# Optimization experiments

Measured on AMD Instinct MI355X. Metric: run time of the kernel, lower is better.

The kernel has to match this reference:

```python
import jax, jax.numpy as jnp
import numpy as np

MARGIN = 0.3


def setup_inputs() -> dict:
    key = jax.random.key(0)
    k1, k2 = jax.random.split(key)
    embeddings = jax.random.normal(k1, (4096, 128), dtype=jnp.float32)
    labels = jax.random.randint(k2, (4096,), 0, 256, dtype=jnp.int64)
    return {"embeddings": embeddings, "labels": labels}


def reference(embeddings, labels):
    # L2-normalize rows (same as F.normalize(p=2, dim=1), eps=1e-12)
    norm = jnp.maximum(jnp.linalg.norm(embeddings, axis=1, keepdims=True), 1e-12)
    e = embeddings / norm
    # cosine distance matrix [N, N]
    dist = 1.0 - e @ e.T

    same = labels[None, :] == labels[:, None]          # [N, N]
    n = labels.shape[0]
    eye = jnp.eye(n, dtype=bool)
    pos_mask = same & ~eye                             # positives excl. self
    neg_mask = ~same

    # dist in [0, 2]; finite sentinels keep max/min well-defined per row
    hardest_pos = jnp.max(jnp.where(pos_mask, dist, -1.0), axis=1)
    hardest_neg = jnp.min(jnp.where(neg_mask, dist, 3.0), axis=1)

    valid = jnp.any(pos_mask, axis=1) & jnp.any(neg_mask, axis=1)
    per_row = jax.nn.relu(hardest_pos - hardest_neg + MARGIN)
    loss_sum = jnp.sum(jnp.where(valid, per_row, 0.0))
    count = jnp.sum(valid)
    return loss_sum / jnp.maximum(count, 1).astype(loss_sum.dtype)
```

## Files before the change

### kernel.cpp

```cpp
#include <hip/hip_runtime.h>
#include <stdint.h>

typedef __bf16 bf16x8 __attribute__((ext_vector_type(8)));
typedef float f32x4 __attribute__((ext_vector_type(4)));

#define N_ROWS 4096
#define KD 128
#define BM 64
#define NCHUNK 16
#define CHUNK 256
#define NBLOCKS (64 * NCHUNK)

__device__ __forceinline__ unsigned short f32_to_bf16_rne(float f) {
    union { float f; uint32_t u; } v; v.f = f;
    uint32_t u = v.u;
    return (unsigned short)((u + 0x7FFFu + ((u >> 16) & 1u)) >> 16);
}

__device__ __forceinline__ int swz(int row, int c) { return row * 16 + (c ^ (row & 15)); }
__device__ __forceinline__ int swzL(int L) { return (L & ~15) | ((L & 15) ^ ((L >> 4) & 15)); }

__global__ __launch_bounds__(256) void normalize_kernel(const float* __restrict__ E,
                                                        unsigned short* __restrict__ out) {
    const int wave = threadIdx.x >> 6;
    const int lane = threadIdx.x & 63;
    const int row = blockIdx.x * 4 + wave;
    const float2 v = *(const float2*)&E[row * KD + lane * 2];
    float s = v.x * v.x + v.y * v.y;
#pragma unroll
    for (int m = 1; m < 64; m <<= 1) s += __shfl_xor(s, m, 64);
    float inv = 0.0f;
    if (s > 0.0f) {
        inv = rsqrtf(s);
        inv = inv * (1.5f - 0.5f * s * inv * inv);
    }
    const unsigned short a = f32_to_bf16_rne(v.x * inv);
    const unsigned short b = f32_to_bf16_rne(v.y * inv);
    ((uint32_t*)out)[row * (KD / 2) + lane] = ((uint32_t)b << 16) | a;
}

__global__ __launch_bounds__(256, 2) void gram_kernel(const unsigned short* __restrict__ Ebits,
                                                      const int* __restrict__ labels,
                                                      float2* __restrict__ partials) {
    __shared__ uint4 Bs4[CHUNK * (KD / 8)];
    __shared__ int ljs[CHUNK];

    const int tid = threadIdx.x;
    const int itile = blockIdx.x & 63;
    const int chunk = blockIdx.x >> 6;
    const int ibase = itile * BM;
    const int cbase = chunk * CHUNK;

    const int wave = tid >> 6, lane = tid & 63;
    const int quad = lane >> 4, l15 = lane & 15;
    const int igb = ibase + wave * 16 + quad * 4;

    uint4 breg[16];
    {
        const uint4* bsrc = (const uint4*)(Ebits + (size_t)cbase * KD);
#pragma unroll
        for (int it = 0; it < 16; ++it) breg[it] = bsrc[it * 256 + tid];
    }
    ljs[tid] = labels[cbase + tid];

    bf16x8 afrag[4];
    {
        const uint4* asrc = (const uint4*)Ebits;
        const int arow = ibase + wave * 16 + l15;
#pragma unroll
        for (int s = 0; s < 4; ++s) afrag[s] = *(const bf16x8*)&asrc[arow * 16 + s * 4 + quad];
    }
    int li_lab[4];
#pragma unroll
    for (int r = 0; r < 4; ++r) li_lab[r] = labels[igb + r];

#pragma unroll
    for (int it = 0; it < 16; ++it) Bs4[swzL(it * 256 + tid)] = breg[it];
    __syncthreads();

    float minpos[4] = {2.0f, 2.0f, 2.0f, 2.0f};
    float maxneg[4] = {-2.0f, -2.0f, -2.0f, -2.0f};

#pragma unroll 4
    for (int t = 0; t < 16; ++t) {
        f32x4 acc = {0.f, 0.f, 0.f, 0.f};
#pragma unroll
        for (int s = 0; s < 4; ++s) {
            const bf16x8 bfrag = *(const bf16x8*)&Bs4[swz(t * 16 + l15, s * 4 + quad)];
            acc = __builtin_amdgcn_mfma_f32_16x16x32_bf16(afrag[s], bfrag, acc, 0, 0, 0);
        }
        const int jg = cbase + t * 16 + l15;
        const int lj = ljs[t * 16 + l15];
#pragma unroll
        for (int r = 0; r < 4; ++r) {
            const float d = acc[r];
            const bool same = (lj == li_lab[r]);
            const float dp = (same && (igb + r != jg)) ? d : 2.0f;
            const float dn = same ? -2.0f : d;
            minpos[r] = fminf(minpos[r], dp);
            maxneg[r] = fmaxf(maxneg[r], dn);
        }
    }

#pragma unroll
    for (int m = 1; m < 16; m <<= 1) {
#pragma unroll
        for (int r = 0; r < 4; ++r) {
            minpos[r] = fminf(minpos[r], __shfl_xor(minpos[r], m, 64));
            maxneg[r] = fmaxf(maxneg[r], __shfl_xor(maxneg[r], m, 64));
        }
    }
    if (l15 == 0) {
#pragma unroll
        for (int r = 0; r < 4; ++r)
            partials[(igb + r) * NCHUNK + chunk] = make_float2(minpos[r], maxneg[r]);
    }
}

__global__ __launch_bounds__(256) void finalize_kernel(const float2* __restrict__ partials,
                                                       float* __restrict__ out) {
    __shared__ float ssum[4];
    __shared__ int scnt[4];
    float sum = 0.f;
    int cnt = 0;
    for (int row = threadIdx.x; row < N_ROWS; row += 256) {
        float mp = 2.f, mn = -2.f;
        const float4* p4 = (const float4*)&partials[row * NCHUNK];
#pragma unroll
        for (int c = 0; c < NCHUNK / 2; ++c) {
            const float4 v = p4[c];
            mp = fminf(mp, fminf(v.x, v.z));
            mn = fmaxf(mn, fmaxf(v.y, v.w));
        }
        if (mp < 1.5f && mn > -1.5f) {
            sum += fmaxf(0.f, mn - mp + 0.3f);
            cnt += 1;
        }
    }
#pragma unroll
    for (int m = 1; m < 64; m <<= 1) {
        sum += __shfl_xor(sum, m, 64);
        cnt += __shfl_xor(cnt, m, 64);
    }
    const int wave = threadIdx.x >> 6, lane = threadIdx.x & 63;
    if (lane == 0) { ssum[wave] = sum; scnt[wave] = cnt; }
    __syncthreads();
    if (threadIdx.x == 0) {
        const float S = ssum[0] + ssum[1] + ssum[2] + ssum[3];
        const int C = scnt[0] + scnt[1] + scnt[2] + scnt[3];
        out[0] = S / (float)(C > 0 ? C : 1);
    }
}

extern "C" void kernel_launch(void* const* d_in, const int* in_sizes, int n_in,
                              void* d_out, int out_size, void* d_ws, size_t ws_size,
                              hipStream_t stream) {
    const float* E = (const float*)d_in[0];
    const int* labels = (const int*)d_in[1];

    unsigned short* ebits = (unsigned short*)d_ws;
    float2* partials = (float2*)((char*)d_ws + (size_t)N_ROWS * KD * 2);
    float* out = (float*)d_out;

    normalize_kernel<<<N_ROWS / 4, 256, 0, stream>>>(E, ebits);
    gram_kernel<<<NBLOCKS, 256, 0, stream>>>(ebits, labels, partials);
    finalize_kernel<<<1, 256, 0, stream>>>(partials, out);
}
```

Baseline: 83.51 us.

## Tile gram B-chunk through small LDS buffer and parallelize finalize across blocks

The gram kernel now stages the A tile in LDS and streams the 256-row B chunk in four 64-row sub-tiles through a smaller shared buffer, replacing the 64KB register-staged chunk. This cuts LDS use per block and register pressure, so more blocks can be resident, at the cost of extra barriers and no overlap between loads and MFMAs. The finalize step moves from a single block to 64 blocks. Each block reduces its rows and combines results through global atomics, and a ticket counter lets the last block write the mean. The atomic counters are reset in the normalize kernel.

```diff
diff --git a/kernel.cpp b/kernel.cpp
--- a/kernel.cpp
+++ b/kernel.cpp
@@ -7,9 +7,12 @@
 #define N_ROWS 4096
 #define KD 128
 #define BM 64
+#define BN 64
 #define NCHUNK 16
 #define CHUNK 256
+#define JT (CHUNK / BN)
 #define NBLOCKS (64 * NCHUNK)
+#define FIN_BLOCKS 64
 
 __device__ __forceinline__ unsigned short f32_to_bf16_rne(float f) {
     union { float f; uint32_t u; } v; v.f = f;
@@ -21,7 +24,13 @@
 __device__ __forceinline__ int swzL(int L) { return (L & ~15) | ((L & 15) ^ ((L >> 4) & 15)); }
 
 __global__ __launch_bounds__(256) void normalize_kernel(const float* __restrict__ E,
-                                                        unsigned short* __restrict__ out) {
+                                                        unsigned short* __restrict__ out,
+                                                        float* __restrict__ gsum,
+                                                        unsigned* __restrict__ gcnt,
+                                                        unsigned* __restrict__ ticket) {
+    if (blockIdx.x == 0 && threadIdx.x == 0) {
+        *gsum = 0.0f; *gcnt = 0u; *ticket = 0u;
+    }
     const int wave = threadIdx.x >> 6;
     const int lane = threadIdx.x & 63;
     const int row = blockIdx.x * 4 + wave;
@@ -39,10 +48,11 @@
     ((uint32_t*)out)[row * (KD / 2) + lane] = ((uint32_t)b << 16) | a;
 }
 
-__global__ __launch_bounds__(256, 2) void gram_kernel(const unsigned short* __restrict__ Ebits,
-                                                      const int* __restrict__ labels,
-                                                      float2* __restrict__ partials) {
-    __shared__ uint4 Bs4[CHUNK * (KD / 8)];
+__global__ __launch_bounds__(256) void gram_kernel(const unsigned short* __restrict__ Ebits,
+                                                   const int* __restrict__ labels,
+                                                   float2* __restrict__ partials) {
+    __shared__ uint4 As4[BM * KD / 8];
+    __shared__ uint4 Bs4[BN * KD / 8];
     __shared__ int ljs[CHUNK];
 
     const int tid = threadIdx.x;
@@ -51,54 +61,65 @@
     const int ibase = itile * BM;
     const int cbase = chunk * CHUNK;
 
+    {
+        const uint4* src = (const uint4*)(Ebits + (size_t)ibase * KD);
+#pragma unroll
+        for (int it = 0; it < 4; ++it) {
+            const int L = it * 256 + tid;
+            As4[swzL(L)] = src[L];
+        }
+        ljs[tid] = labels[cbase + tid];
+    }
+    __syncthreads();
+
     const int wave = tid >> 6, lane = tid & 63;
     const int quad = lane >> 4, l15 = lane & 15;
     const int igb = ibase + wave * 16 + quad * 4;
 
-    uint4 breg[16];
-    {
-        const uint4* bsrc = (const uint4*)(Ebits + (size_t)cbase * KD);
-#pragma unroll
-        for (int it = 0; it < 16; ++it) breg[it] = bsrc[it * 256 + tid];
-    }
-    ljs[tid] = labels[cbase + tid];
-
     bf16x8 afrag[4];
-    {
-        const uint4* asrc = (const uint4*)Ebits;
-        const int arow = ibase + wave * 16 + l15;
-#pragma unroll
-        for (int s = 0; s < 4; ++s) afrag[s] = *(const bf16x8*)&asrc[arow * 16 + s * 4 + quad];
-    }
+#pragma unroll
+    for (int s = 0; s < 4; ++s)
+        afrag[s] = *(const bf16x8*)&As4[swz(wave * 16 + l15, s * 4 + quad)];
+
     int li_lab[4];
 #pragma unroll
     for (int r = 0; r < 4; ++r) li_lab[r] = labels[igb + r];
-
-#pragma unroll
-    for (int it = 0; it < 16; ++it) Bs4[swzL(it * 256 + tid)] = breg[it];
-    __syncthreads();
 
     float minpos[4] = {2.0f, 2.0f, 2.0f, 2.0f};
     float maxneg[4] = {-2.0f, -2.0f, -2.0f, -2.0f};
 
-#pragma unroll 4
-    for (int t = 0; t < 16; ++t) {
-        f32x4 acc = {0.f, 0.f, 0.f, 0.f};
-#pragma unroll
-        for (int s = 0; s < 4; ++s) {
-            const bf16x8 bfrag = *(const bf16x8*)&Bs4[swz(t * 16 + l15, s * 4 + quad)];
-            acc = __builtin_amdgcn_mfma_f32_16x16x32_bf16(afrag[s], bfrag, acc, 0, 0, 0);
-        }
-        const int jg = cbase + t * 16 + l15;
-        const int lj = ljs[t * 16 + l15];
-#pragma unroll
-        for (int r = 0; r < 4; ++r) {
-            const float d = acc[r];
-            const bool same = (lj == li_lab[r]);
-            const float dp = (same && (igb + r != jg)) ? d : 2.0f;
-            const float dn = same ? -2.0f : d;
-            minpos[r] = fminf(minpos[r], dp);
-            maxneg[r] = fmaxf(maxneg[r], dn);
+    for (int jt = 0; jt < JT; ++jt) {
+        const int jbase = cbase + jt * BN;
+        __syncthreads();
+        {
+            const uint4* src = (const uint4*)(Ebits + (size_t)jbase * KD);
+#pragma unroll
+            for (int it = 0; it < 4; ++it) {
+                const int L = it * 256 + tid;
+                Bs4[swzL(L)] = src[L];
+            }
+        }
+        __syncthreads();
+
+#pragma unroll
+        for (int t = 0; t < 4; ++t) {
+            f32x4 acc = {0.f, 0.f, 0.f, 0.f};
+#pragma unroll
+            for (int s = 0; s < 4; ++s) {
+                const bf16x8 bfrag = *(const bf16x8*)&Bs4[swz(t * 16 + l15, s * 4 + quad)];
+                acc = __builtin_amdgcn_mfma_f32_16x16x32_bf16(afrag[s], bfrag, acc, 0, 0, 0);
+            }
+            const int jg = jbase + t * 16 + l15;
+            const int lj = ljs[jt * BN + t * 16 + l15];
+#pragma unroll
+            for (int r = 0; r < 4; ++r) {
+                const float d = acc[r];
+                const bool same = (lj == li_lab[r]);
+                const float dp = (same && (igb + r != jg)) ? d : 2.0f;
+                const float dn = same ? -2.0f : d;
+                minpos[r] = fminf(minpos[r], dp);
+                maxneg[r] = fmaxf(maxneg[r], dn);
+            }
         }
     }
 
@@ -118,37 +139,50 @@
 }
 
 __global__ __launch_bounds__(256) void finalize_kernel(const float2* __restrict__ partials,
+                                                       float* __restrict__ gsum,
+                                                       unsigned* __restrict__ gcnt,
+                                                       unsigned* __restrict__ ticket,
                                                        float* __restrict__ out) {
     __shared__ float ssum[4];
     __shared__ int scnt[4];
-    float sum = 0.f;
-    int cnt = 0;
-    for (int row = threadIdx.x; row < N_ROWS; row += 256) {
-        float mp = 2.f, mn = -2.f;
-        const float4* p4 = (const float4*)&partials[row * NCHUNK];
-#pragma unroll
-        for (int c = 0; c < NCHUNK / 2; ++c) {
-            const float4 v = p4[c];
-            mp = fminf(mp, fminf(v.x, v.z));
-            mn = fmaxf(mn, fmaxf(v.y, v.w));
-        }
-        if (mp < 1.5f && mn > -1.5f) {
-            sum += fmaxf(0.f, mn - mp + 0.3f);
-            cnt += 1;
-        }
+    __shared__ unsigned s_old;
+
+    const int tid = threadIdx.x;
+    const int sub = tid & 3;
+    const int row = blockIdx.x * 64 + (tid >> 2);
+
+    const float4* p4 = (const float4*)&partials[row * NCHUNK];
+    const float4 a = p4[sub * 2];
+    const float4 b = p4[sub * 2 + 1];
+    float mp = fminf(fminf(a.x, a.z), fminf(b.x, b.z));
+    float mn = fmaxf(fmaxf(a.y, a.w), fmaxf(b.y, b.w));
+    mp = fminf(mp, __shfl_xor(mp, 1, 64)); mp = fminf(mp, __shfl_xor(mp, 2, 64));
+    mn = fmaxf(mn, __shfl_xor(mn, 1, 64)); mn = fmaxf(mn, __shfl_xor(mn, 2, 64));
+
+    float sum = 0.f; int cnt = 0;
+    if (sub == 0 && mp < 1.5f && mn > -1.5f) {
+        sum = fmaxf(0.f, mn - mp + 0.3f);
+        cnt = 1;
     }
 #pragma unroll
     for (int m = 1; m < 64; m <<= 1) {
         sum += __shfl_xor(sum, m, 64);
         cnt += __shfl_xor(cnt, m, 64);
     }
-    const int wave = threadIdx.x >> 6, lane = threadIdx.x & 63;
+    const int wave = tid >> 6, lane = tid & 63;
     if (lane == 0) { ssum[wave] = sum; scnt[wave] = cnt; }
     __syncthreads();
-    if (threadIdx.x == 0) {
-        const float S = ssum[0] + ssum[1] + ssum[2] + ssum[3];
-        const int C = scnt[0] + scnt[1] + scnt[2] + scnt[3];
-        out[0] = S / (float)(C > 0 ? C : 1);
+    if (tid == 0) {
+        atomicAdd(gsum, ssum[0] + ssum[1] + ssum[2] + ssum[3]);
+        atomicAdd(gcnt, (unsigned)(scnt[0] + scnt[1] + scnt[2] + scnt[3]));
+    }
+    __syncthreads();
+    if (tid == 0) s_old = atomicAdd(ticket, 1u);
+    __syncthreads();
+    if (s_old == (unsigned)(FIN_BLOCKS - 1) && tid == 0) {
+        const float S = __hip_atomic_load(gsum, __ATOMIC_RELAXED, __HIP_MEMORY_SCOPE_AGENT);
+        const unsigned C = __hip_atomic_load(gcnt, __ATOMIC_RELAXED, __HIP_MEMORY_SCOPE_AGENT);
+        out[0] = S / (float)(C > 0u ? C : 1u);
     }
 }
 
@@ -160,9 +194,12 @@
 
     unsigned short* ebits = (unsigned short*)d_ws;
     float2* partials = (float2*)((char*)d_ws + (size_t)N_ROWS * KD * 2);
+    float* gsum = (float*)(partials + N_ROWS * NCHUNK);
+    unsigned* gcnt = (unsigned*)(gsum + 1);
+    unsigned* ticket = gcnt + 1;
     float* out = (float*)d_out;
 
-    normalize_kernel<<<N_ROWS / 4, 256, 0, stream>>>(E, ebits);
+    normalize_kernel<<<N_ROWS / 4, 256, 0, stream>>>(E, ebits, gsum, gcnt, ticket);
     gram_kernel<<<NBLOCKS, 256, 0, stream>>>(ebits, labels, partials);
-    finalize_kernel<<<1, 256, 0, stream>>>(partials, out);
-}
+    finalize_kernel<<<FIN_BLOCKS, 256, 0, stream>>>(partials, gsum, gcnt, ticket, out);
+}
```

After: 74.46 us. 10.8% less time.
